# Kernel tuning notes

Measured on AMD Instinct MI355X. Metric: run time of the kernel, lower is better.

The kernel has to match this reference:

```python
import jax, jax.numpy as jnp
import numpy as np

B, N = 128, 196
ENC, DEC, ATT = 2048, 512, 512

def setup_inputs() -> dict:
    key = jax.random.key(0)
    ks = jax.random.split(key, 8)
    s_enc = 1.0 / np.sqrt(ENC)
    s_dec = 1.0 / np.sqrt(DEC)
    s_att = 1.0 / np.sqrt(ATT)
    return {
        "encoder_out": jax.random.normal(ks[0], (B, N, ENC), jnp.float32),
        "decoder_hidden": jax.random.normal(ks[1], (B, DEC), jnp.float32),
        "W_enc": jax.random.uniform(ks[2], (ENC, ATT), jnp.float32, -s_enc, s_enc),
        "b_enc": jax.random.uniform(ks[3], (ATT,), jnp.float32, -s_enc, s_enc),
        "W_dec": jax.random.uniform(ks[4], (DEC, ATT), jnp.float32, -s_dec, s_dec),
        "b_dec": jax.random.uniform(ks[5], (ATT,), jnp.float32, -s_dec, s_dec),
        "W_full": jax.random.uniform(ks[6], (ATT,), jnp.float32, -s_att, s_att),
        "b_full": jax.random.uniform(ks[7], (), jnp.float32, -s_att, s_att),
    }

def reference(encoder_out, decoder_hidden, W_enc, b_enc, W_dec, b_dec, W_full, b_full):
    # att1: [B, N, ATT]; att2: [B, 1, ATT]
    att1 = jnp.einsum('bne,ea->bna', encoder_out, W_enc) + b_enc
    att2 = decoder_hidden @ W_dec + b_dec
    combined = jax.nn.relu(att1 + att2[:, None, :])
    e = jnp.einsum('bna,a->bn', combined, W_full) + b_full  # [B, N]
    alpha = jax.nn.softmax(e, axis=1)
    attention_weighted_encoding = jnp.einsum('bne,bn->be', encoder_out, alpha)
    return attention_weighted_encoding, alpha
```

## Files before the change

### kernel.cpp

```cpp
#include <hip/hip_runtime.h>
#include <hip/hip_bf16.h>

#define BB   128
#define NN   196
#define MM   (BB*NN)
#define ENC  2048
#define ATT  512
#define DEC  512
#define BK   32
#define KSTEPS (ENC/BK)
#define BM   128
#define BA   256

using f32x4 = __attribute__((ext_vector_type(4))) float;
using s16x8 = __attribute__((ext_vector_type(8))) short;
using u16x4 = __attribute__((ext_vector_type(4))) unsigned short;
using u16x8 = __attribute__((ext_vector_type(8))) unsigned short;

__device__ __forceinline__ short f2bf(float f) {
    union { __hip_bfloat16 h; short s; } u;
    u.h = __float2bfloat16(f);
    return u.s;
}
__device__ __forceinline__ float bf2f(unsigned short u) {
    union { unsigned int i; float f; } v;
    v.i = ((unsigned int)u) << 16;
    return v.f;
}

__global__ void transpose_convert_kernel(const float* __restrict__ W,
                                         unsigned short* __restrict__ Wt) {
    __shared__ float tile[32][33];
    const int a0 = blockIdx.x * 32;
    const int k0 = blockIdx.y * 32;
    const int tx = threadIdx.x & 31, ty = threadIdx.x >> 5;
    #pragma unroll
    for (int i = 0; i < 32; i += 8)
        tile[ty + i][tx] = W[(size_t)(k0 + ty + i) * ATT + a0 + tx];
    __syncthreads();
    #pragma unroll
    for (int i = 0; i < 32; i += 8) {
        union { __hip_bfloat16 h; unsigned short u; } v;
        v.h = __float2bfloat16(tile[tx][ty + i]);
        Wt[(size_t)(a0 + ty + i) * ENC + k0 + tx] = v.u;
    }
}

__global__ __launch_bounds__(256)
void enc_cvt_kernel(const float* __restrict__ enc,
                    unsigned short* __restrict__ encb) {
    const size_t row = blockIdx.x;
    const int t = threadIdx.x;
    const float* in = enc + row * ENC + t * 8;
    f32x4 a = *(const f32x4*)in;
    f32x4 b = *(const f32x4*)(in + 4);
    u16x8 o;
    #pragma unroll
    for (int j = 0; j < 4; ++j) {
        o[j]     = (unsigned short)f2bf(a[j]);
        o[4 + j] = (unsigned short)f2bf(b[j]);
    }
    *(u16x8*)(encb + row * ENC + t * 8) = o;
}

__global__ void att2_kernel(const float* __restrict__ dec,
                            const float* __restrict__ Wd,
                            const float* __restrict__ bd,
                            const float* __restrict__ benc,
                            float* __restrict__ att2) {
    const int b  = blockIdx.x;
    const int c0 = blockIdx.y * 64;
    const int t  = threadIdx.x;
    const int cl = t & 63, kg = t >> 6;
    __shared__ float sdec[DEC];
    __shared__ float red[4][64];
    sdec[t]       = dec[b * DEC + t];
    sdec[t + 256] = dec[b * DEC + t + 256];
    __syncthreads();
    float acc = 0.f;
    const float* wp = Wd + c0 + cl;
    #pragma unroll 8
    for (int k = kg * 128; k < kg * 128 + 128; ++k)
        acc += sdec[k] * wp[(size_t)k * ATT];
    red[kg][cl] = acc;
    __syncthreads();
    if (t < 64) {
        float s = red[0][t] + red[1][t] + red[2][t] + red[3][t];
        att2[b * ATT + c0 + t] = s + bd[c0 + t] + benc[c0 + t];
    }
}

__global__ __launch_bounds__(512, 4)
void gemm_bf16_kernel(const unsigned short* __restrict__ encb,
                      const unsigned short* __restrict__ Wt,
                      const float* __restrict__ att2,
                      const float* __restrict__ Wf,
                      float* __restrict__ e_part) {
    __shared__ unsigned short sA[512 * 8];
    __shared__ unsigned short sB[1024 * 8];
    __shared__ float e_sm[BM];

    const int t    = threadIdx.x;
    const int lane = t & 63;
    const int w    = t >> 6;
    const int wm   = w >> 2;
    const int wa   = w & 3;
    const int aBlk  = blockIdx.x;
    const int mBase = blockIdx.y * BM;
    const int aBase = aBlk * BA;
    const int r = lane & 15, q = lane >> 4;

    if (t < BM) e_sm[t] = 0.f;

    const unsigned short* gA =
        encb + (size_t)(mBase + ((t >> 6) << 4) + (t & 15)) * ENC + ((t >> 4) & 3) * 8;
    const unsigned short* gB[2];
    #pragma unroll
    for (int i = 0; i < 2; ++i) {
        int s = i * 512 + t;
        gB[i] = Wt + (size_t)(aBase + ((s >> 6) << 4) + (s & 15)) * ENC + ((s >> 4) & 3) * 8;
    }

    f32x4 acc[4][4] = {};

    #pragma unroll 1
    for (int ks = 0; ks < KSTEPS; ++ks) {
        __builtin_amdgcn_global_load_lds(
            (const __attribute__((address_space(1))) void*)(gA + (size_t)ks * BK),
            (__attribute__((address_space(3))) void*)((char*)sA + t * 16),
            16, 0, 0);
        #pragma unroll
        for (int i = 0; i < 2; ++i)
            __builtin_amdgcn_global_load_lds(
                (const __attribute__((address_space(1))) void*)(gB[i] + (size_t)ks * BK),
                (__attribute__((address_space(3))) void*)((char*)sB + (i * 512 + t) * 16),
                16, 0, 0);
        __syncthreads();

        s16x8 af[4], bf[4];
        #pragma unroll
        for (int mi = 0; mi < 4; ++mi)
            af[mi] = *(const s16x8*)((const char*)sA + (((wm * 4 + mi) * 64 + lane) * 16));
        #pragma unroll
        for (int ni = 0; ni < 4; ++ni)
            bf[ni] = *(const s16x8*)((const char*)sB + (((wa * 4 + ni) * 64 + lane) * 16));
        #pragma unroll
        for (int mi = 0; mi < 4; ++mi)
            #pragma unroll
            for (int ni = 0; ni < 4; ++ni)
                acc[mi][ni] = __builtin_amdgcn_mfma_f32_16x16x32_bf16(
                    af[mi], bf[ni], acc[mi][ni], 0, 0, 0);
        __syncthreads();
    }

    float wfv[4];
    #pragma unroll
    for (int ni = 0; ni < 4; ++ni)
        wfv[ni] = Wf[aBase + wa * 64 + ni * 16 + r];

    #pragma unroll
    for (int mi = 0; mi < 4; ++mi) {
        #pragma unroll
        for (int reg = 0; reg < 4; ++reg) {
            int lrow = wm * 64 + mi * 16 + q * 4 + reg;
            int gm = mBase + lrow;
            int b = gm / NN;
            const float* a2 = att2 + b * ATT + aBase + wa * 64;
            float rs = 0.f;
            #pragma unroll
            for (int ni = 0; ni < 4; ++ni) {
                float v = acc[mi][ni][reg] + a2[ni * 16 + r];
                rs += fmaxf(v, 0.f) * wfv[ni];
            }
            rs += __shfl_xor(rs, 1);
            rs += __shfl_xor(rs, 2);
            rs += __shfl_xor(rs, 4);
            rs += __shfl_xor(rs, 8);
            if (r == 0) atomicAdd(&e_sm[lrow], rs);
        }
    }
    __syncthreads();
    if (t < BM)
        e_part[(size_t)aBlk * MM + mBase + t] = e_sm[t];
}

__global__ __launch_bounds__(256, 5)
void gemm_e_kernel(const float* __restrict__ enc,
                   const unsigned short* __restrict__ Wt,
                   const float* __restrict__ att2,
                   const float* __restrict__ Wf,
                   float* __restrict__ e_part) {
    __shared__ float sA[64 * 32];
    __shared__ unsigned short sB[128 * 32];
    __shared__ float e_sm[64];

    const int t    = threadIdx.x;
    const int lane = t & 63;
    const int w    = t >> 6;
    const int aBlk  = blockIdx.x;
    const int mBase = blockIdx.y * 64;
    const int aBase = aBlk * 128;
    const int r = lane & 15, q = lane >> 4;

    const float* gA[2];
    #pragma unroll
    for (int i = 0; i < 2; ++i) {
        int s = i * 256 + t;
        int row = s >> 3, ck = s & 7;
        int g = ck ^ (row & 7);
        gA[i] = enc + (size_t)(mBase + row) * ENC + g * 4;
    }
    const unsigned short* gB[2];
    #pragma unroll
    for (int i = 0; i < 2; ++i) {
        int s = i * 256 + t;
        int row = s >> 2, ck = s & 3;
        int g = ck ^ ((row & 3) ^ ((row >> 2) & 3));
        gB[i] = Wt + (size_t)(aBase + row) * ENC + g * 8;
    }

    int offA[4][2];
    #pragma unroll
    for (int mi = 0; mi < 4; ++mi) {
        int row = mi * 16 + r;
        offA[mi][0] = row * 128 + ((2 * q)     ^ (row & 7)) * 16;
        offA[mi][1] = row * 128 + ((2 * q + 1) ^ (row & 7)) * 16;
    }
    int offB[2];
    #pragma unroll
    for (int ni = 0; ni < 2; ++ni) {
        int col = w * 32 + ni * 16 + r;
        offB[ni] = col * 64 + (q ^ ((col & 3) ^ ((col >> 2) & 3))) * 16;
    }

    f32x4 acc[4][2] = {};

    #pragma unroll 1
    for (int ks = 0; ks < KSTEPS; ++ks) {
        #pragma unroll
        for (int i = 0; i < 2; ++i)
            __builtin_amdgcn_global_load_lds(
                (const __attribute__((address_space(1))) void*)(gA[i] + (size_t)ks * BK),
                (__attribute__((address_space(3))) void*)((char*)sA + (i * 256 + w * 64) * 16),
                16, 0, 0);
        #pragma unroll
        for (int i = 0; i < 2; ++i)
            __builtin_amdgcn_global_load_lds(
                (const __attribute__((address_space(1))) void*)(gB[i] + (size_t)ks * BK),
                (__attribute__((address_space(3))) void*)((char*)sB + (i * 256 + w * 64) * 16),
                16, 0, 0);
        __syncthreads();

        s16x8 af[4], bf[2];
        #pragma unroll
        for (int mi = 0; mi < 4; ++mi) {
            f32x4 f0 = *(const f32x4*)((const char*)sA + offA[mi][0]);
            f32x4 f1 = *(const f32x4*)((const char*)sA + offA[mi][1]);
            s16x8 a;
            #pragma unroll
            for (int j = 0; j < 4; ++j) { a[j] = f2bf(f0[j]); a[4 + j] = f2bf(f1[j]); }
            af[mi] = a;
        }
        #pragma unroll
        for (int ni = 0; ni < 2; ++ni)
            bf[ni] = *(const s16x8*)((const char*)sB + offB[ni]);

        #pragma unroll
        for (int mi = 0; mi < 4; ++mi)
            #pragma unroll
            for (int ni = 0; ni < 2; ++ni)
                acc[mi][ni] = __builtin_amdgcn_mfma_f32_16x16x32_bf16(
                    af[mi], bf[ni], acc[mi][ni], 0, 0, 0);
        __syncthreads();
    }

    if (t < 64) e_sm[t] = 0.f;
    __syncthreads();

    float wfv[2];
    #pragma unroll
    for (int ni = 0; ni < 2; ++ni)
        wfv[ni] = Wf[aBase + w * 32 + ni * 16 + r];

    #pragma unroll
    for (int mi = 0; mi < 4; ++mi) {
        #pragma unroll
        for (int reg = 0; reg < 4; ++reg) {
            int lrow = mi * 16 + q * 4 + reg;
            int gm = mBase + lrow;
            int b = gm / NN;
            const float* a2 = att2 + b * ATT + aBase + w * 32;
            float rs = 0.f;
            #pragma unroll
            for (int ni = 0; ni < 2; ++ni) {
                float v = acc[mi][ni][reg] + a2[ni * 16 + r];
                rs += fmaxf(v, 0.f) * wfv[ni];
            }
            rs += __shfl_xor(rs, 1);
            rs += __shfl_xor(rs, 2);
            rs += __shfl_xor(rs, 4);
            rs += __shfl_xor(rs, 8);
            if (r == 0) atomicAdd(&e_sm[lrow], rs);
        }
    }
    __syncthreads();
    if (t < 64)
        e_part[(size_t)aBlk * MM + mBase + t] = e_sm[t];
}

__global__ void softmax_kernel(const float* __restrict__ e_part,
                               const float* __restrict__ b_full,
                               float* __restrict__ out,
                               float* __restrict__ alpha_ws,
                               int nparts) {
    const int b = blockIdx.x;
    const int t = threadIdx.x;
    __shared__ float sm[256];

    float v = -3.0e38f;
    if (t < NN) {
        int gm = b * NN + t;
        float s = b_full[0];
        for (int p = 0; p < nparts; ++p) s += e_part[(size_t)p * MM + gm];
        v = s;
    }
    sm[t] = v;
    __syncthreads();
    for (int s = 128; s > 0; s >>= 1) {
        if (t < s) sm[t] = fmaxf(sm[t], sm[t + s]);
        __syncthreads();
    }
    float mx = sm[0];
    __syncthreads();
    float ex = (t < NN) ? __expf(v - mx) : 0.f;
    sm[t] = ex;
    __syncthreads();
    for (int s = 128; s > 0; s >>= 1) {
        if (t < s) sm[t] += sm[t + s];
        __syncthreads();
    }
    float inv = 1.0f / sm[0];
    if (t < NN) {
        float a = ex * inv;
        out[BB * ENC + b * NN + t] = a;
        alpha_ws[b * NN + t] = a;
    }
}

__global__ __launch_bounds__(256)
void awe_bf16_kernel(const unsigned short* __restrict__ encb,
                     const float* __restrict__ alpha_ws,
                     float* __restrict__ out) {
    const int b = blockIdx.x, chunk = blockIdx.y;
    const int t = threadIdx.x;
    __shared__ float al[NN];
    if (t < NN) al[t] = alpha_ws[b * NN + t];
    __syncthreads();

    const unsigned short* ep = encb + (size_t)b * NN * ENC + chunk * 1024 + t * 4;
    f32x4 acc0 = {}, acc1 = {}, acc2 = {}, acc3 = {};
    #pragma unroll 2
    for (int n = 0; n < NN; n += 4) {
        u16x4 v0 = *(const u16x4*)(ep + (size_t)(n + 0) * ENC);
        u16x4 v1 = *(const u16x4*)(ep + (size_t)(n + 1) * ENC);
        u16x4 v2 = *(const u16x4*)(ep + (size_t)(n + 2) * ENC);
        u16x4 v3 = *(const u16x4*)(ep + (size_t)(n + 3) * ENC);
        #pragma unroll
        for (int j = 0; j < 4; ++j) {
            acc0[j] += bf2f(v0[j]) * al[n];
            acc1[j] += bf2f(v1[j]) * al[n + 1];
            acc2[j] += bf2f(v2[j]) * al[n + 2];
            acc3[j] += bf2f(v3[j]) * al[n + 3];
        }
    }
    f32x4 s = (acc0 + acc1) + (acc2 + acc3);
    *(f32x4*)(out + (size_t)b * ENC + chunk * 1024 + t * 4) = s;
}

__global__ __launch_bounds__(256)
void awe_kernel(const float* __restrict__ enc,
                const float* __restrict__ alpha_ws,
                float* __restrict__ out) {
    const int b = blockIdx.x, chunk = blockIdx.y;
    const int t = threadIdx.x;
    __shared__ float al[NN];
    if (t < NN) al[t] = alpha_ws[b * NN + t];
    __syncthreads();

    const float* ep = enc + (size_t)b * NN * ENC + chunk * 1024 + t * 4;
    f32x4 acc0 = {}, acc1 = {}, acc2 = {}, acc3 = {};
    #pragma unroll 2
    for (int n = 0; n < NN; n += 4) {
        f32x4 v0 = *(const f32x4*)(ep + (size_t)(n + 0) * ENC);
        f32x4 v1 = *(const f32x4*)(ep + (size_t)(n + 1) * ENC);
        f32x4 v2 = *(const f32x4*)(ep + (size_t)(n + 2) * ENC);
        f32x4 v3 = *(const f32x4*)(ep + (size_t)(n + 3) * ENC);
        acc0 += v0 * al[n];
        acc1 += v1 * al[n + 1];
        acc2 += v2 * al[n + 2];
        acc3 += v3 * al[n + 3];
    }
    f32x4 s = (acc0 + acc1) + (acc2 + acc3);
    *(f32x4*)(out + (size_t)b * ENC + chunk * 1024 + t * 4) = s;
}

extern "C" void kernel_launch(void* const* d_in, const int* in_sizes, int n_in,
                              void* d_out, int out_size, void* d_ws, size_t ws_size,
                              hipStream_t stream) {
    const float* enc    = (const float*)d_in[0];
    const float* dec    = (const float*)d_in[1];
    const float* W_enc  = (const float*)d_in[2];
    const float* b_enc  = (const float*)d_in[3];
    const float* W_dec  = (const float*)d_in[4];
    const float* b_dec  = (const float*)d_in[5];
    const float* W_full = (const float*)d_in[6];
    const float* b_full = (const float*)d_in[7];
    float* out = (float*)d_out;

    char* ws = (char*)d_ws;
    unsigned short* Wt = (unsigned short*)ws;
    float* att2     = (float*)(ws + 2097152);
    float* e_part   = (float*)(ws + 2359296);
    float* alpha_ws = (float*)(ws + 2760704);
    unsigned short* encb = (unsigned short*)(ws + 3145728);
    const size_t WS_NEED = 3145728 + (size_t)MM * ENC * 2;

    transpose_convert_kernel<<<dim3(ATT / 32, ENC / 32), 256, 0, stream>>>(W_enc, Wt);
    att2_kernel<<<dim3(BB, 8), 256, 0, stream>>>(dec, W_dec, b_dec, b_enc, att2);

    if (ws_size >= WS_NEED) {
        enc_cvt_kernel<<<MM, 256, 0, stream>>>(enc, encb);
        gemm_bf16_kernel<<<dim3(ATT / BA, MM / BM), 512, 0, stream>>>(encb, Wt, att2, W_full, e_part);
        softmax_kernel<<<BB, 256, 0, stream>>>(e_part, b_full, out, alpha_ws, 2);
        awe_bf16_kernel<<<dim3(BB, 2), 256, 0, stream>>>(encb, alpha_ws, out);
    } else {
        gemm_e_kernel<<<dim3(4, MM / 64), 256, 0, stream>>>(enc, Wt, att2, W_full, e_part);
        softmax_kernel<<<BB, 256, 0, stream>>>(e_part, b_full, out, alpha_ws, 4);
        awe_kernel<<<dim3(BB, 2), 256, 0, stream>>>(enc, alpha_ws, out);
    }
}
```

Before: 440.4 us.

## Double-buffer LDS tiles in bf16 GEMM to overlap global loads with MFMA

Splits the shared-memory A and B tiles into two ping-pong buffers. The load for the next K step is issued before the MFMA work on the current buffer, and one barrier per step replaces the previous two. This is meant to hide global-to-LDS latency behind compute. In exchange, LDS use per block doubles, which may cut occupancy, and correctness relies on the async global_load_lds completing before the barrier.

New measurement: 439.9 us. About the same (-0.1%).

```diff
diff --git a/kernel.cpp b/kernel.cpp
--- a/kernel.cpp
+++ b/kernel.cpp
@@ -96,8 +96,10 @@
                       const float* __restrict__ att2,
                       const float* __restrict__ Wf,
                       float* __restrict__ e_part) {
-    __shared__ unsigned short sA[512 * 8];
-    __shared__ unsigned short sB[1024 * 8];
+    __shared__ unsigned short sA0[512 * 8];
+    __shared__ unsigned short sA1[512 * 8];
+    __shared__ unsigned short sB0[1024 * 8];
+    __shared__ unsigned short sB1[1024 * 8];
     __shared__ float e_sm[BM];
 
     const int t    = threadIdx.x;
@@ -123,35 +125,50 @@
 
     f32x4 acc[4][4] = {};
 
-    #pragma unroll 1
-    for (int ks = 0; ks < KSTEPS; ++ks) {
+    auto stage = [&](unsigned short* bA, unsigned short* bB, int ks) {
         __builtin_amdgcn_global_load_lds(
             (const __attribute__((address_space(1))) void*)(gA + (size_t)ks * BK),
-            (__attribute__((address_space(3))) void*)((char*)sA + t * 16),
+            (__attribute__((address_space(3))) void*)((char*)bA + t * 16),
             16, 0, 0);
         #pragma unroll
         for (int i = 0; i < 2; ++i)
             __builtin_amdgcn_global_load_lds(
                 (const __attribute__((address_space(1))) void*)(gB[i] + (size_t)ks * BK),
-                (__attribute__((address_space(3))) void*)((char*)sB + (i * 512 + t) * 16),
+                (__attribute__((address_space(3))) void*)((char*)bB + (i * 512 + t) * 16),
                 16, 0, 0);
-        __syncthreads();
-
+    };
+
+    auto compute = [&](const unsigned short* bA, const unsigned short* bB) {
         s16x8 af[4], bf[4];
         #pragma unroll
         for (int mi = 0; mi < 4; ++mi)
-            af[mi] = *(const s16x8*)((const char*)sA + (((wm * 4 + mi) * 64 + lane) * 16));
+            af[mi] = *(const s16x8*)((const char*)bA + (((wm * 4 + mi) * 64 + lane) * 16));
         #pragma unroll
         for (int ni = 0; ni < 4; ++ni)
-            bf[ni] = *(const s16x8*)((const char*)sB + (((wa * 4 + ni) * 64 + lane) * 16));
+            bf[ni] = *(const s16x8*)((const char*)bB + (((wa * 4 + ni) * 64 + lane) * 16));
         #pragma unroll
         for (int mi = 0; mi < 4; ++mi)
             #pragma unroll
             for (int ni = 0; ni < 4; ++ni)
                 acc[mi][ni] = __builtin_amdgcn_mfma_f32_16x16x32_bf16(
                     af[mi], bf[ni], acc[mi][ni], 0, 0, 0);
-        __syncthreads();
-    }
+    };
+
+    stage(sA0, sB0, 0);
+    __syncthreads();
+    #pragma unroll 1
+    for (int ks = 0; ks < KSTEPS - 2; ks += 2) {
+        stage(sA1, sB1, ks + 1);
+        compute(sA0, sB0);
+        __syncthreads();
+        stage(sA0, sB0, ks + 2);
+        compute(sA1, sB1);
+        __syncthreads();
+    }
+    stage(sA1, sB1, KSTEPS - 1);
+    compute(sA0, sB0);
+    __syncthreads();
+    compute(sA1, sB1);
 
     float wfv[4];
     #pragma unroll
```
